# Kernel tuning notes

Measured on AMD Instinct MI355X. Metric: run time of the kernel, lower is better.

Reference implementation:

```python
import jax, jax.numpy as jnp
import numpy as np

N_NODES = 50000
N_GRAPHS = 100
NODES_PER_GRAPH = 500
N_EDGES = 800000
EMB = 128
N_LAYERS = 4
Z_DIM = 2 * EMB + 1  # [x_i, x_j, dist]
BN_EPS = 1e-5


def setup_inputs() -> dict:
    key = jax.random.key(0)
    ks = jax.random.split(key, 12)
    z = jax.random.randint(ks[0], (N_NODES,), 0, 100)
    pos = jax.random.normal(ks[1], (N_NODES, 3), dtype=jnp.float32) * 3.0
    batch = jnp.repeat(jnp.arange(N_GRAPHS), NODES_PER_GRAPH)
    # within-graph random edges (stands in for radius_graph's bounded-degree output)
    rng = np.random.default_rng(0)
    eg = np.repeat(np.arange(N_GRAPHS), N_EDGES // N_GRAPHS)
    src = eg * NODES_PER_GRAPH + rng.integers(0, NODES_PER_GRAPH, N_EDGES)
    dst = eg * NODES_PER_GRAPH + rng.integers(0, NODES_PER_GRAPH, N_EDGES)
    edge_index = jnp.asarray(np.stack([src, dst]), dtype=jnp.int64)
    s = 0.05
    emb = jax.random.normal(ks[2], (100, EMB), dtype=jnp.float32)
    Wf = jax.random.normal(ks[3], (N_LAYERS, Z_DIM, EMB), dtype=jnp.float32) * s
    bf = jnp.zeros((N_LAYERS, EMB), dtype=jnp.float32)
    Ws = jax.random.normal(ks[4], (N_LAYERS, Z_DIM, EMB), dtype=jnp.float32) * s
    bs = jnp.zeros((N_LAYERS, EMB), dtype=jnp.float32)
    bn1_g = jnp.ones((N_LAYERS, EMB), dtype=jnp.float32)
    bn1_b = jnp.zeros((N_LAYERS, EMB), dtype=jnp.float32)
    bn2_g = jnp.ones((N_LAYERS, EMB), dtype=jnp.float32)
    bn2_b = jnp.zeros((N_LAYERS, EMB), dtype=jnp.float32)
    W1 = jax.random.normal(ks[5], (EMB, EMB), dtype=jnp.float32) * s
    b1 = jnp.zeros((EMB,), dtype=jnp.float32)
    W2 = jax.random.normal(ks[6], (EMB, 1), dtype=jnp.float32) * s
    b2 = jnp.zeros((1,), dtype=jnp.float32)
    return {"pos": pos, "emb": emb, "Wf": Wf, "bf": bf, "Ws": Ws, "bs": bs,
            "bn1_g": bn1_g, "bn1_b": bn1_b, "bn2_g": bn2_g, "bn2_b": bn2_b,
            "W1": W1, "b1": b1, "W2": W2, "b2": b2,
            "z": z, "batch": batch, "edge_index": edge_index}


def _batchnorm(x, g, b):
    mu = jnp.mean(x, axis=0)
    var = jnp.var(x, axis=0)  # biased, matches torch BN training normalization
    return (x - mu) * jax.lax.rsqrt(var + BN_EPS) * g + b


def reference(pos, emb, Wf, bf, Ws, bs, bn1_g, bn1_b, bn2_g, bn2_b, W1, b1, W2, b2, z, batch, edge_index):
    j, i = edge_index[0], edge_index[1]  # source j -> target i (PyG flow)
    x = emb[z]  # [N, EMB]
    dist = jnp.linalg.norm(pos[i] - pos[j], axis=-1, keepdims=True)  # [E, 1]
    for l in range(N_LAYERS):
        zc = jnp.concatenate([x[i], x[j], dist], axis=-1)  # [E, 257]
        msg = jax.nn.sigmoid(zc @ Wf[l] + bf[l]) * jax.nn.softplus(zc @ Ws[l] + bs[l])
        agg = jax.ops.segment_sum(msg, i, num_segments=N_NODES)  # CGConv 'add' aggregation
        out = _batchnorm(agg, bn1_g[l], bn1_b[l]) + x  # CGConv internal BN + residual
        x = jax.nn.relu(_batchnorm(out, bn2_g[l], bn2_b[l]))  # outer BN + ReLU (dropout=0)
    # global mean pool over graphs
    gsum = jax.ops.segment_sum(x, batch, num_segments=N_GRAPHS)
    cnt = jax.ops.segment_sum(jnp.ones((N_NODES, 1), x.dtype), batch, num_segments=N_GRAPHS)
    g = gsum / cnt
    h = jax.nn.relu(g @ W1 + b1)
    return (h @ W2 + b2).reshape(-1)  # [N_GRAPHS]
```

## Files before the change

kernel.cpp:

```cpp
#include <hip/hip_runtime.h>

#define NN 50000
#define NG 100
#define NPG 500
#define NE 800000
#define EPG 8000
#define EMBD 128
#define NL 4
#define CS_BLOCKS 1000
#define CS_ROWS 50

typedef __attribute__((ext_vector_type(8))) short short8v;
typedef __attribute__((ext_vector_type(4))) float float4v;
typedef __attribute__((ext_vector_type(2))) float f2;

__device__ __forceinline__ unsigned short f2bf(float v) {
  unsigned u = __float_as_uint(v);
  u += 0x7FFFu + ((u >> 16) & 1u);
  return (unsigned short)(u >> 16);
}
__device__ __forceinline__ float bf2f(unsigned short h) {
  return __uint_as_float(((unsigned)h) << 16);
}

__device__ __forceinline__ float fexp2(float x) {
#if __has_builtin(__builtin_amdgcn_exp2f)
  return __builtin_amdgcn_exp2f(x);
#else
  float r; asm("v_exp_f32 %0, %1" : "=v"(r) : "v"(x)); return r;
#endif
}
__device__ __forceinline__ float flog2(float x) {
#if __has_builtin(__builtin_amdgcn_logf)
  return __builtin_amdgcn_logf(x);
#else
  float r; asm("v_log_f32 %0, %1" : "=v"(r) : "v"(x)); return r;
#endif
}
__device__ __forceinline__ float frcp(float x) {
#if __has_builtin(__builtin_amdgcn_rcpf)
  return __builtin_amdgcn_rcpf(x);
#else
  float r; asm("v_rcp_f32 %0, %1" : "=v"(r) : "v"(x)); return r;
#endif
}

__device__ __forceinline__ f2 unpk(unsigned v) {
  f2 r;
  r.x = __uint_as_float(v << 16);
  r.y = __uint_as_float(v & 0xffff0000u);
  return r;
}

__global__ void prep_w(const float* __restrict__ Wf, const float* __restrict__ Ws,
                       unsigned short* __restrict__ whT) {
  int idx = blockIdx.x * 256 + threadIdx.x;
  int k = idx & 127;
  int oc = (idx >> 7) & 511;
  int l = idx >> 16;
  const float* W;
  int row, c;
  if (oc < 128) { W = Wf; row = k; c = oc; }
  else if (oc < 256) { W = Ws; row = k; c = oc - 128; }
  else {
    int t = oc - 256;
    int p = t >> 2, r = t & 3;
    c = 2 * p + (r & 1);
    W = (r < 2) ? Wf : Ws;
    row = 128 + k;
  }
  whT[idx] = f2bf(W[(size_t)l * 32896 + (size_t)row * 128 + c]);
}

__global__ void gather_x(const float* __restrict__ emb, const int* __restrict__ z,
                         unsigned short* __restrict__ xh) {
  const int total = NN * 32;
  for (int idx = blockIdx.x * 256 + threadIdx.x; idx < total; idx += gridDim.x * 256) {
    int n = idx >> 5, c4 = (idx & 31) * 4;
    float4 v = *(const float4*)(emb + (size_t)z[n] * EMBD + c4);
    ushort4 h;
    h.x = f2bf(v.x); h.y = f2bf(v.y); h.z = f2bf(v.z); h.w = f2bf(v.w);
    *(ushort4*)(xh + (size_t)idx * 4) = h;
  }
}

__global__ __launch_bounds__(512) void csr_build(const int* __restrict__ ei,
                                                 const float* __restrict__ pos,
                                                 int* __restrict__ offs, int* __restrict__ deg,
                                                 uint2* __restrict__ csr) {
  __shared__ int hist[NPG];
  __shared__ int scan[512];
  const int g = blockIdx.x, t = threadIdx.x;
  const int nbase = g * NPG;
  const int e0 = g * EPG;
  for (int n = t; n < NPG; n += 512) hist[n] = 0;
  __syncthreads();
  for (int e = t; e < EPG; e += 512) atomicAdd(&hist[ei[NE + e0 + e] - nbase], 1);
  __syncthreads();
  int v = (t < NPG) ? hist[t] : 0;
  scan[t] = v;
  __syncthreads();
  for (int d = 1; d < 512; d <<= 1) {
    int a = (t >= d) ? scan[t - d] : 0;
    __syncthreads();
    scan[t] += a;
    __syncthreads();
  }
  if (t < NPG) {
    int off = scan[t] - v;
    offs[nbase + t] = e0 + off;
    deg[nbase + t] = v;
    hist[t] = off;
  }
  __syncthreads();
  for (int e = t; e < EPG; e += 512) {
    int j = ei[e0 + e];
    int i = ei[NE + e0 + e];
    float dx = pos[i * 3 + 0] - pos[j * 3 + 0];
    float dy = pos[i * 3 + 1] - pos[j * 3 + 1];
    float dz = pos[i * 3 + 2] - pos[j * 3 + 2];
    float dist = sqrtf(dx * dx + dy * dy + dz * dz);
    int p = atomicAdd(&hist[i - nbase], 1);
    csr[e0 + p] = make_uint2((unsigned)j, __float_as_uint(dist));
  }
}

#define BM 128
#define BN 128
__global__ __launch_bounds__(256, 2) void gemm_proj(const unsigned short* __restrict__ xh,
                                                    const unsigned short* __restrict__ whT,
                                                    unsigned short* __restrict__ P, int l) {
  __shared__ __align__(16) unsigned short smem[32768];
  unsigned short* sA = smem;
  unsigned short* sB = smem + 16384;
  const int tid = threadIdx.x;
  const int R0 = blockIdx.x * BM;
  const int C0 = blockIdx.y * BN;
  for (int gid = tid; gid < BM * 16; gid += 256) {
    int row = gid >> 4, gc = gid & 15;
    int grow = R0 + row;
    uint4 v = make_uint4(0u, 0u, 0u, 0u);
    if (grow < NN) v = *(const uint4*)(xh + (size_t)grow * 128 + gc * 8);
    int gs = (gc & 8) | ((gc ^ row) & 7);
    *(uint4*)((char*)sA + row * 256 + gs * 16) = v;
  }
  for (int gid = tid; gid < BN * 16; gid += 256) {
    int c = gid >> 4, gc = gid & 15;
    uint4 v = *(const uint4*)(whT + ((size_t)l * 512 + C0 + c) * 128 + gc * 8);
    int gs = (gc & 8) | ((gc ^ c) & 7);
    *(uint4*)((char*)sB + c * 256 + gs * 16) = v;
  }
  __syncthreads();
  const int w = tid >> 6, lane = tid & 63;
  const int lr = lane & 15, lk = lane >> 4;
  float4v acc[2][8];
#pragma unroll
  for (int i = 0; i < 2; i++)
#pragma unroll
    for (int j = 0; j < 8; j++) acc[i][j] = (float4v){0.f, 0.f, 0.f, 0.f};
#pragma unroll
  for (int kb = 0; kb < 4; kb++) {
    int g = kb * 4 + lk;
    short8v a[2], b[8];
#pragma unroll
    for (int rf = 0; rf < 2; rf++) {
      int row = w * 32 + rf * 16 + lr;
      int gs = (g & 8) | ((g ^ row) & 7);
      a[rf] = *(const short8v*)((const char*)sA + row * 256 + gs * 16);
    }
#pragma unroll
    for (int cf = 0; cf < 8; cf++) {
      int c = cf * 16 + lr;
      int gs = (g & 8) | ((g ^ c) & 7);
      b[cf] = *(const short8v*)((const char*)sB + c * 256 + gs * 16);
    }
#pragma unroll
    for (int rf = 0; rf < 2; rf++)
#pragma unroll
      for (int cf = 0; cf < 8; cf++)
        acc[rf][cf] = __builtin_amdgcn_mfma_f32_16x16x32_bf16(a[rf], b[cf], acc[rf][cf], 0, 0, 0);
  }
  __syncthreads();
  unsigned short* sC = smem;
#pragma unroll
  for (int rf = 0; rf < 2; rf++) {
#pragma unroll
    for (int cf = 0; cf < 8; cf++) {
      int col = cf * 16 + lr;
#pragma unroll
      for (int j = 0; j < 4; j++) {
        int row = w * 32 + rf * 16 + lk * 4 + j;
        sC[row * 136 + col] = f2bf(acc[rf][cf][j]);
      }
    }
  }
  __syncthreads();
  for (int it = tid; it < BM * 16; it += 256) {
    int row = it >> 4, gc = it & 15;
    int grow = R0 + row;
    if (grow < NN) {
      uint4 v = *(const uint4*)(sC + row * 136 + gc * 8);
      *(uint4*)(P + (size_t)grow * 512 + C0 + gc * 8) = v;
    }
  }
}

__global__ __launch_bounds__(256) void edge_gather(const unsigned short* __restrict__ P,
                                                   const uint2* __restrict__ csr,
                                                   const int* __restrict__ offs,
                                                   const int* __restrict__ deg,
                                                   const float* __restrict__ Wf,
                                                   const float* __restrict__ bf,
                                                   const float* __restrict__ Ws,
                                                   const float* __restrict__ bs,
                                                   float* __restrict__ agg, int l) {
  const float L = 1.4426950408889634f;
  const float LN2 = 0.6931471805599453f;
  const int lane = threadIdx.x & 63;
  const int wid = __builtin_amdgcn_readfirstlane(threadIdx.x >> 6);
  const int bid = blockIdx.x;
  const int xcd = bid & 7, bidx = bid >> 3;
  const int wg = (xcd < 4) ? xcd * 1563 + bidx : 4 * 1563 + (xcd - 4) * 1562 + bidx;
  const int i = wg * 4 + wid;
  const int f0 = lane * 2;

  const unsigned* Piu = (const unsigned*)(P + (size_t)i * 512);
  unsigned pif = Piu[lane];
  unsigned pis = Piu[64 + lane];

  float2 wfd = *(const float2*)(Wf + (size_t)l * 32896 + 256 * 128 + f0);
  float2 wsd = *(const float2*)(Ws + (size_t)l * 32896 + 256 * 128 + f0);
  float2 bfv = *(const float2*)(bf + l * 128 + f0);
  float2 bsv = *(const float2*)(bs + l * 128 + f0);

  f2 bflv, bslv, wflv, wslv;
  {
    f2 pi_f = unpk(pif), pi_s = unpk(pis);
    bflv.x = (pi_f.x + bfv.x) * L; bflv.y = (pi_f.y + bfv.y) * L;
    bslv.x = (pi_s.x + bsv.x) * L; bslv.y = (pi_s.y + bsv.y) * L;
    wflv.x = wfd.x * L; wflv.y = wfd.y * L;
    wslv.x = wsd.x * L; wslv.y = wsd.y * L;
  }

  const int off = __builtin_amdgcn_readfirstlane(offs[i]);
  const int nd = __builtin_amdgcn_readfirstlane(deg[i]);
  const uint2* ep = csr + off;
  f2 acc = (f2){0.f, 0.f};

#define EDGE_BODY(DVU, V)                                          \
  {                                                                \
    float dv = __uint_as_float(DVU);                               \
    f2 pf = unpk((V).x) * L + (bflv + dv * wflv);                  \
    f2 ps = unpk((V).y) * L + (bslv + dv * wslv);                  \
    f2 a, b, r, lg;                                                \
    a.x = fexp2(-pf.x); a.y = fexp2(-pf.y);                        \
    b.x = fexp2(ps.x);  b.y = fexp2(ps.y);                         \
    r.x = frcp(a.x + 1.f); r.y = frcp(a.y + 1.f);                  \
    lg.x = flog2(b.x + 1.f); lg.y = flog2(b.y + 1.f);              \
    acc += r * lg;                                                 \
  }

  for (int k = 0; k < nd; k += 8) {
    const int rem = nd - k;
    int le = lane & 7;
    if (le >= rem) le = rem - 1;
    uint2 ed = ep[k + le];
    unsigned js[8], ds[8];
#pragma unroll
    for (int e = 0; e < 8; e++) {
      js[e] = __builtin_amdgcn_readlane(ed.x, e);
      ds[e] = __builtin_amdgcn_readlane(ed.y, e);
    }
    uint2 v[8];
#pragma unroll
    for (int e = 0; e < 8; e++)
      v[e] = ((const uint2*)(P + (size_t)js[e] * 512))[64 + lane];
#pragma unroll
    for (int e = 0; e < 8; e++)
      if (e < rem) EDGE_BODY(ds[e], v[e])
  }
#undef EDGE_BODY

  acc.x *= LN2; acc.y *= LN2;
  *(f2*)(agg + (size_t)i * EMBD + f0) = acc;
}

__global__ __launch_bounds__(256) void col_stats(const float* __restrict__ agg,
                                                 const unsigned short* __restrict__ xh,
                                                 float* __restrict__ partial) {
  const int b = blockIdx.x, tid = threadIdx.x;
  const int c4 = tid & 31;
  const int h = tid >> 5;
  const int r0 = b * CS_ROWS;
  float4 sa = {0, 0, 0, 0}, sa2 = {0, 0, 0, 0}, sx = {0, 0, 0, 0}, sx2 = {0, 0, 0, 0},
         sax = {0, 0, 0, 0};
  for (int rr = h; rr < CS_ROWS; rr += 8) {
    size_t idx = (size_t)(r0 + rr) * EMBD + c4 * 4;
    float4 a = *(const float4*)(agg + idx);
    ushort4 hx = *(const ushort4*)(xh + idx);
    float x0 = bf2f(hx.x), x1 = bf2f(hx.y), x2 = bf2f(hx.z), x3 = bf2f(hx.w);
    sa.x += a.x; sa.y += a.y; sa.z += a.z; sa.w += a.w;
    sa2.x += a.x * a.x; sa2.y += a.y * a.y; sa2.z += a.z * a.z; sa2.w += a.w * a.w;
    sx.x += x0; sx.y += x1; sx.z += x2; sx.w += x3;
    sx2.x += x0 * x0; sx2.y += x1 * x1; sx2.z += x2 * x2; sx2.w += x3 * x3;
    sax.x += a.x * x0; sax.y += a.y * x1; sax.z += a.z * x2; sax.w += a.w * x3;
  }
  __shared__ float4 sm[256];
  float* p = partial + (size_t)b * 640;
#define REDUCE_STAT(V, OUTOFF)                                              \
  sm[tid] = V;                                                              \
  __syncthreads();                                                          \
  if (h == 0) {                                                             \
    float4 s = sm[tid];                                                     \
    for (int g = 1; g < 8; g++) {                                           \
      float4 o = sm[g * 32 + tid];                                          \
      s.x += o.x; s.y += o.y; s.z += o.z; s.w += o.w;                       \
    }                                                                       \
    *(float4*)(p + (OUTOFF) + c4 * 4) = s;                                  \
  }                                                                         \
  __syncthreads();
  REDUCE_STAT(sa, 0)
  REDUCE_STAT(sa2, 128)
  REDUCE_STAT(sx, 256)
  REDUCE_STAT(sx2, 384)
  REDUCE_STAT(sax, 512)
#undef REDUCE_STAT
}

__global__ __launch_bounds__(256) void bn_fold(const float* __restrict__ partial,
                                               const float* __restrict__ bn1g,
                                               const float* __restrict__ bn1b,
                                               const float* __restrict__ bn2g,
                                               const float* __restrict__ bn2b,
                                               float* __restrict__ abc, int l) {
  __shared__ float sm[5 * 256];
  const int t = threadIdx.x;
  const int ci = t & 15;
  const int col = blockIdx.x * 16 + ci;
  const int chunk = t >> 4;
  float s0 = 0, s1 = 0, s2 = 0, s3 = 0, s4 = 0;
  for (int b = chunk; b < CS_BLOCKS; b += 16) {
    const float* p = partial + (size_t)b * 640 + col;
    s0 += p[0]; s1 += p[128]; s2 += p[256]; s3 += p[384]; s4 += p[512];
  }
  sm[t] = s0; sm[256 + t] = s1; sm[512 + t] = s2; sm[768 + t] = s3; sm[1024 + t] = s4;
  __syncthreads();
  if (t < 16) {
    int c = blockIdx.x * 16 + t;
    float a0 = 0, a1 = 0, a2 = 0, a3 = 0, a4 = 0;
    for (int ch = 0; ch < 16; ch++) {
      int u = ch * 16 + t;
      a0 += sm[u]; a1 += sm[256 + u]; a2 += sm[512 + u]; a3 += sm[768 + u]; a4 += sm[1024 + u];
    }
    const double Ninv = 1.0 / (double)NN;
    double Ea = a0 * Ninv, Ea2 = a1 * Ninv, Ex = a2 * Ninv, Ex2 = a3 * Ninv, Eax = a4 * Ninv;
    double var1 = Ea2 - Ea * Ea;
    double g1 = bn1g[l * 128 + c], b1 = bn1b[l * 128 + c];
    double g2 = bn2g[l * 128 + c], b2v = bn2b[l * 128 + c];
    double s1d = g1 / sqrt(var1 + 1e-5);
    double t1 = b1 - Ea * s1d;
    double mu_o = s1d * Ea + t1 + Ex;
    double Eo2 = s1d * s1d * Ea2 + 2.0 * s1d * t1 * Ea + t1 * t1 + 2.0 * (s1d * Eax + t1 * Ex) + Ex2;
    double var_o = Eo2 - mu_o * mu_o;
    double s2d = g2 / sqrt(var_o + 1e-5);
    double t2 = b2v - mu_o * s2d;
    abc[c] = (float)(s1d * s2d);
    abc[128 + c] = (float)s2d;
    abc[256 + c] = (float)(t1 * s2d + t2);
  }
}

__global__ void fuse_bn(const float* __restrict__ agg, unsigned short* __restrict__ xh,
                        const float* __restrict__ abc) {
  const int total = NN * 32;
  for (int idx = blockIdx.x * 256 + threadIdx.x; idx < total; idx += gridDim.x * 256) {
    int c4 = (idx & 31) * 4;
    size_t base = (size_t)idx * 4;
    float4 a = *(const float4*)(agg + base);
    ushort4 hx = *(const ushort4*)(xh + base);
    float4 A = *(const float4*)(abc + c4);
    float4 B = *(const float4*)(abc + 128 + c4);
    float4 C = *(const float4*)(abc + 256 + c4);
    float4 o;
    o.x = fmaxf(fmaf(A.x, a.x, fmaf(B.x, bf2f(hx.x), C.x)), 0.f);
    o.y = fmaxf(fmaf(A.y, a.y, fmaf(B.y, bf2f(hx.y), C.y)), 0.f);
    o.z = fmaxf(fmaf(A.z, a.z, fmaf(B.z, bf2f(hx.z), C.z)), 0.f);
    o.w = fmaxf(fmaf(A.w, a.w, fmaf(B.w, bf2f(hx.w), C.w)), 0.f);
    ushort4 hh;
    hh.x = f2bf(o.x); hh.y = f2bf(o.y); hh.z = f2bf(o.z); hh.w = f2bf(o.w);
    *(ushort4*)(xh + base) = hh;
  }
}

__global__ __launch_bounds__(512) void pool_mlp(const unsigned short* __restrict__ xh,
                                                const float* __restrict__ W1,
                                                const float* __restrict__ b1,
                                                const float* __restrict__ W2,
                                                const float* __restrict__ b2,
                                                float* __restrict__ out) {
  __shared__ float red[512];
  __shared__ float gl[128];
  const int g = blockIdx.x, t = threadIdx.x;
  const int c = t & 127, q = t >> 7;
  const unsigned short* bx = xh + (size_t)g * NPG * EMBD;
  float s = 0.f;
  for (int r = q; r < NPG; r += 4) s += bf2f(bx[(size_t)r * EMBD + c]);
  red[t] = s;
  __syncthreads();
  if (q == 0) gl[c] = (red[c] + red[128 + c] + red[256 + c] + red[384 + c]) * (1.f / NPG);
  __syncthreads();
  float acc = 0.f;
  for (int k = q * 32; k < q * 32 + 32; k++) acc = fmaf(gl[k], W1[k * EMBD + c], acc);
  red[t] = acc;
  __syncthreads();
  if (q == 0) {
    float h = fmaxf(red[c] + red[128 + c] + red[256 + c] + red[384 + c] + b1[c], 0.f);
    red[c] = h * W2[c];
  }
  __syncthreads();
  for (int sft = 64; sft > 0; sft >>= 1) {
    if (t < sft) red[t] += red[t + sft];
    __syncthreads();
  }
  if (t == 0) out[g] = red[0] + b2[0];
}

extern "C" void kernel_launch(void* const* d_in, const int* in_sizes, int n_in,
                              void* d_out, int out_size, void* d_ws, size_t ws_size,
                              hipStream_t stream) {
  const float* pos = (const float*)d_in[0];
  const float* emb = (const float*)d_in[1];
  const float* Wf = (const float*)d_in[2];
  const float* bf = (const float*)d_in[3];
  const float* Ws = (const float*)d_in[4];
  const float* bs = (const float*)d_in[5];
  const float* bn1g = (const float*)d_in[6];
  const float* bn1b = (const float*)d_in[7];
  const float* bn2g = (const float*)d_in[8];
  const float* bn2b = (const float*)d_in[9];
  const float* W1 = (const float*)d_in[10];
  const float* b1 = (const float*)d_in[11];
  const float* W2 = (const float*)d_in[12];
  const float* b2 = (const float*)d_in[13];
  const int* z = (const int*)d_in[14];
  const int* ei = (const int*)d_in[16];
  float* out = (float*)d_out;

  char* ws = (char*)d_ws;
  unsigned short* xh = (unsigned short*)(ws + 0);
  unsigned short* P = (unsigned short*)(ws + 12800000);
  float* agg = (float*)(ws + 64000000);
  uint2* csr = (uint2*)(ws + 89600000);
  int* deg = (int*)(ws + 96000000);
  int* offs = (int*)(ws + 96200000);
  unsigned short* whT = (unsigned short*)(ws + 96400000);
  float* partial = (float*)(ws + 96924288);
  float* abc = (float*)(ws + 99484288);

  prep_w<<<1024, 256, 0, stream>>>(Wf, Ws, whT);
  gather_x<<<2048, 256, 0, stream>>>(emb, z, xh);
  csr_build<<<NG, 512, 0, stream>>>(ei, pos, offs, deg, csr);
  for (int l = 0; l < NL; l++) {
    gemm_proj<<<dim3(391, 4), 256, 0, stream>>>(xh, whT, P, l);
    edge_gather<<<NN / 4, 256, 0, stream>>>(P, csr, offs, deg, Wf, bf, Ws, bs, agg, l);
    col_stats<<<CS_BLOCKS, 256, 0, stream>>>(agg, xh, partial);
    bn_fold<<<8, 256, 0, stream>>>(partial, bn1g, bn1b, bn2g, bn2b, abc, l);
    fuse_bn<<<2048, 256, 0, stream>>>(agg, xh, abc);
  }
  pool_mlp<<<NG, 512, 0, stream>>>(xh, W1, b1, W2, b2, out);
}
```

Baseline: 581.0 us.

## Store aggregates in bf16, simplify edge loop, reorder GEMM grid

The per-node aggregate buffer becomes bf16 instead of fp32, which halves its write traffic in edge_gather and its read traffic in col_stats and fuse_bn. The edge loop now unrolls 4 edges at a time, with scalar reads of each CSR entry taking the place of the lane-distributed readlane scheme and its masked tail. The GEMM grid is transposed so the four column tiles of a row block launch next to each other, which should improve reuse of the A tile in cache. Rounding the aggregates to bf16 before batch-norm statistics adds some numerical error.

Result: faster. 540.0 us (-7.1%).

```diff
diff --git a/kernel.cpp b/kernel.cpp
--- a/kernel.cpp
+++ b/kernel.cpp
@@ -134,8 +134,8 @@
   unsigned short* sA = smem;
   unsigned short* sB = smem + 16384;
   const int tid = threadIdx.x;
-  const int R0 = blockIdx.x * BM;
-  const int C0 = blockIdx.y * BN;
+  const int R0 = blockIdx.y * BM;
+  const int C0 = blockIdx.x * BN;
   for (int gid = tid; gid < BM * 16; gid += 256) {
     int row = gid >> 4, gc = gid & 15;
     int grow = R0 + row;
@@ -213,7 +213,7 @@
                                                    const float* __restrict__ bf,
                                                    const float* __restrict__ Ws,
                                                    const float* __restrict__ bs,
-                                                   float* __restrict__ agg, int l) {
+                                                   unsigned short* __restrict__ aggh, int l) {
   const float L = 1.4426950408889634f;
   const float LN2 = 0.6931471805599453f;
   const int lane = threadIdx.x & 63;
@@ -260,32 +260,41 @@
     acc += r * lg;                                                 \
   }
 
-  for (int k = 0; k < nd; k += 8) {
-    const int rem = nd - k;
-    int le = lane & 7;
-    if (le >= rem) le = rem - 1;
-    uint2 ed = ep[k + le];
-    unsigned js[8], ds[8];
-#pragma unroll
-    for (int e = 0; e < 8; e++) {
-      js[e] = __builtin_amdgcn_readlane(ed.x, e);
-      ds[e] = __builtin_amdgcn_readlane(ed.y, e);
-    }
-    uint2 v[8];
-#pragma unroll
-    for (int e = 0; e < 8; e++)
-      v[e] = ((const uint2*)(P + (size_t)js[e] * 512))[64 + lane];
-#pragma unroll
-    for (int e = 0; e < 8; e++)
-      if (e < rem) EDGE_BODY(ds[e], v[e])
+  int k = 0;
+  for (; k + 3 < nd; k += 4) {
+    uint2 e0 = ep[k], e1 = ep[k + 1], e2 = ep[k + 2], e3 = ep[k + 3];
+    unsigned j0 = __builtin_amdgcn_readfirstlane(e0.x);
+    unsigned j1 = __builtin_amdgcn_readfirstlane(e1.x);
+    unsigned j2 = __builtin_amdgcn_readfirstlane(e2.x);
+    unsigned j3 = __builtin_amdgcn_readfirstlane(e3.x);
+    unsigned d0 = __builtin_amdgcn_readfirstlane(e0.y);
+    unsigned d1 = __builtin_amdgcn_readfirstlane(e1.y);
+    unsigned d2 = __builtin_amdgcn_readfirstlane(e2.y);
+    unsigned d3 = __builtin_amdgcn_readfirstlane(e3.y);
+    uint2 v0 = ((const uint2*)(P + (size_t)j0 * 512))[64 + lane];
+    uint2 v1 = ((const uint2*)(P + (size_t)j1 * 512))[64 + lane];
+    uint2 v2 = ((const uint2*)(P + (size_t)j2 * 512))[64 + lane];
+    uint2 v3 = ((const uint2*)(P + (size_t)j3 * 512))[64 + lane];
+    EDGE_BODY(d0, v0)
+    EDGE_BODY(d1, v1)
+    EDGE_BODY(d2, v2)
+    EDGE_BODY(d3, v3)
+  }
+  for (; k < nd; k++) {
+    uint2 e0 = ep[k];
+    unsigned j0 = __builtin_amdgcn_readfirstlane(e0.x);
+    unsigned d0 = __builtin_amdgcn_readfirstlane(e0.y);
+    uint2 v0 = ((const uint2*)(P + (size_t)j0 * 512))[64 + lane];
+    EDGE_BODY(d0, v0)
   }
 #undef EDGE_BODY
 
   acc.x *= LN2; acc.y *= LN2;
-  *(f2*)(agg + (size_t)i * EMBD + f0) = acc;
-}
-
-__global__ __launch_bounds__(256) void col_stats(const float* __restrict__ agg,
+  unsigned packed = ((unsigned)f2bf(acc.y) << 16) | (unsigned)f2bf(acc.x);
+  ((unsigned*)(aggh + (size_t)i * EMBD))[lane] = packed;
+}
+
+__global__ __launch_bounds__(256) void col_stats(const unsigned short* __restrict__ aggh,
                                                  const unsigned short* __restrict__ xh,
                                                  float* __restrict__ partial) {
   const int b = blockIdx.x, tid = threadIdx.x;
@@ -296,14 +305,15 @@
          sax = {0, 0, 0, 0};
   for (int rr = h; rr < CS_ROWS; rr += 8) {
     size_t idx = (size_t)(r0 + rr) * EMBD + c4 * 4;
-    float4 a = *(const float4*)(agg + idx);
+    ushort4 ha = *(const ushort4*)(aggh + idx);
     ushort4 hx = *(const ushort4*)(xh + idx);
+    float a0 = bf2f(ha.x), a1 = bf2f(ha.y), a2 = bf2f(ha.z), a3 = bf2f(ha.w);
     float x0 = bf2f(hx.x), x1 = bf2f(hx.y), x2 = bf2f(hx.z), x3 = bf2f(hx.w);
-    sa.x += a.x; sa.y += a.y; sa.z += a.z; sa.w += a.w;
-    sa2.x += a.x * a.x; sa2.y += a.y * a.y; sa2.z += a.z * a.z; sa2.w += a.w * a.w;
+    sa.x += a0; sa.y += a1; sa.z += a2; sa.w += a3;
+    sa2.x += a0 * a0; sa2.y += a1 * a1; sa2.z += a2 * a2; sa2.w += a3 * a3;
     sx.x += x0; sx.y += x1; sx.z += x2; sx.w += x3;
     sx2.x += x0 * x0; sx2.y += x1 * x1; sx2.z += x2 * x2; sx2.w += x3 * x3;
-    sax.x += a.x * x0; sax.y += a.y * x1; sax.z += a.z * x2; sax.w += a.w * x3;
+    sax.x += a0 * x0; sax.y += a1 * x1; sax.z += a2 * x2; sax.w += a3 * x3;
   }
   __shared__ float4 sm[256];
   float* p = partial + (size_t)b * 640;
@@ -370,22 +380,22 @@
   }
 }
 
-__global__ void fuse_bn(const float* __restrict__ agg, unsigned short* __restrict__ xh,
+__global__ void fuse_bn(const unsigned short* __restrict__ aggh, unsigned short* __restrict__ xh,
                         const float* __restrict__ abc) {
   const int total = NN * 32;
   for (int idx = blockIdx.x * 256 + threadIdx.x; idx < total; idx += gridDim.x * 256) {
     int c4 = (idx & 31) * 4;
     size_t base = (size_t)idx * 4;
-    float4 a = *(const float4*)(agg + base);
+    ushort4 ha = *(const ushort4*)(aggh + base);
     ushort4 hx = *(const ushort4*)(xh + base);
     float4 A = *(const float4*)(abc + c4);
     float4 B = *(const float4*)(abc + 128 + c4);
     float4 C = *(const float4*)(abc + 256 + c4);
     float4 o;
-    o.x = fmaxf(fmaf(A.x, a.x, fmaf(B.x, bf2f(hx.x), C.x)), 0.f);
-    o.y = fmaxf(fmaf(A.y, a.y, fmaf(B.y, bf2f(hx.y), C.y)), 0.f);
-    o.z = fmaxf(fmaf(A.z, a.z, fmaf(B.z, bf2f(hx.z), C.z)), 0.f);
-    o.w = fmaxf(fmaf(A.w, a.w, fmaf(B.w, bf2f(hx.w), C.w)), 0.f);
+    o.x = fmaxf(fmaf(A.x, bf2f(ha.x), fmaf(B.x, bf2f(hx.x), C.x)), 0.f);
+    o.y = fmaxf(fmaf(A.y, bf2f(ha.y), fmaf(B.y, bf2f(hx.y), C.y)), 0.f);
+    o.z = fmaxf(fmaf(A.z, bf2f(ha.z), fmaf(B.z, bf2f(hx.z), C.z)), 0.f);
+    o.w = fmaxf(fmaf(A.w, bf2f(ha.w), fmaf(B.w, bf2f(hx.w), C.w)), 0.f);
     ushort4 hh;
     hh.x = f2bf(o.x); hh.y = f2bf(o.y); hh.z = f2bf(o.z); hh.w = f2bf(o.w);
     *(ushort4*)(xh + base) = hh;
@@ -449,23 +459,23 @@
   char* ws = (char*)d_ws;
   unsigned short* xh = (unsigned short*)(ws + 0);
   unsigned short* P = (unsigned short*)(ws + 12800000);
-  float* agg = (float*)(ws + 64000000);
-  uint2* csr = (uint2*)(ws + 89600000);
-  int* deg = (int*)(ws + 96000000);
-  int* offs = (int*)(ws + 96200000);
-  unsigned short* whT = (unsigned short*)(ws + 96400000);
-  float* partial = (float*)(ws + 96924288);
-  float* abc = (float*)(ws + 99484288);
+  unsigned short* aggh = (unsigned short*)(ws + 64000000);
+  uint2* csr = (uint2*)(ws + 76800000);
+  int* deg = (int*)(ws + 83200000);
+  int* offs = (int*)(ws + 83400000);
+  unsigned short* whT = (unsigned short*)(ws + 83600000);
+  float* partial = (float*)(ws + 84124288);
+  float* abc = (float*)(ws + 86684288);
 
   prep_w<<<1024, 256, 0, stream>>>(Wf, Ws, whT);
   gather_x<<<2048, 256, 0, stream>>>(emb, z, xh);
   csr_build<<<NG, 512, 0, stream>>>(ei, pos, offs, deg, csr);
   for (int l = 0; l < NL; l++) {
-    gemm_proj<<<dim3(391, 4), 256, 0, stream>>>(xh, whT, P, l);
-    edge_gather<<<NN / 4, 256, 0, stream>>>(P, csr, offs, deg, Wf, bf, Ws, bs, agg, l);
-    col_stats<<<CS_BLOCKS, 256, 0, stream>>>(agg, xh, partial);
+    gemm_proj<<<dim3(4, 391), 256, 0, stream>>>(xh, whT, P, l);
+    edge_gather<<<NN / 4, 256, 0, stream>>>(P, csr, offs, deg, Wf, bf, Ws, bs, aggh, l);
+    col_stats<<<CS_BLOCKS, 256, 0, stream>>>(aggh, xh, partial);
     bn_fold<<<8, 256, 0, stream>>>(partial, bn1g, bn1b, bn2g, bn2b, abc, l);
-    fuse_bn<<<2048, 256, 0, stream>>>(agg, xh, abc);
+    fuse_bn<<<2048, 256, 0, stream>>>(aggh, xh, abc);
   }
   pool_mlp<<<NG, 512, 0, stream>>>(xh, W1, b1, W2, b2, out);
 }
```
